# Kernel tuning notes

Measured on AMD Instinct MI355X. Metric: run time of the kernel, lower is better.

## Reference

```python
import jax, jax.numpy as jnp
import numpy as np

B, S, H, T, NF = 64, 512, 1024, 4, 12
P = NF * (NF - 1) // 2  # 66 step pairs


def _head(x, w1, b1, w2, b2):
    # LinearsHead (eval mode: dropout = identity): linear -> relu -> linear
    return jax.nn.relu(x @ w1 + b1) @ w2 + b2


def setup_inputs() -> dict:
    key = jax.random.key(0)
    ks = jax.random.split(key, 12)
    sc = 0.02
    # non-overlapping contiguous spans: targets then facts, each L tokens
    L = S // (T + NF)  # 32
    t_start = jnp.arange(T, dtype=jnp.int32) * L
    f_start = (T + jnp.arange(NF, dtype=jnp.int32)) * L
    target_offsets = jnp.broadcast_to(jnp.stack([t_start, t_start + L], -1), (B, T, 2))
    fact_offsets = jnp.broadcast_to(jnp.stack([f_start, f_start + L], -1), (B, NF, 2))
    return {
        'seq_features': jax.random.normal(ks[0], (B, S, H), jnp.float32),
        'cls_features': jax.random.normal(ks[1], (B, H), jnp.float32),
        'target_offsets': target_offsets,
        'fact_offsets': fact_offsets,
        'fact_score_mask': jnp.ones((B, NF, T), jnp.float32),
        'sentsim_w1': sc * jax.random.normal(ks[2], (2 * H, H), jnp.float32),
        'sentsim_b1': jnp.zeros((H,), jnp.float32),
        'sentsim_w2': sc * jax.random.normal(ks[3], (H, 1), jnp.float32),
        'sentsim_b2': jnp.zeros((1,), jnp.float32),
        'step_w1': sc * jax.random.normal(ks[4], (2 * H, H), jnp.float32),
        'step_b1': jnp.zeros((H,), jnp.float32),
        'step_w2': sc * jax.random.normal(ks[5], (H, 1), jnp.float32),
        'step_b2': jnp.zeros((1,), jnp.float32),
        'state_w1': sc * jax.random.normal(ks[6], (H, H), jnp.float32),
        'state_b1': jnp.zeros((H,), jnp.float32),
        'state_w2': sc * jax.random.normal(ks[7], (H, 1), jnp.float32),
        'state_b2': jnp.zeros((1,), jnp.float32),
        'abd_w1': sc * jax.random.normal(ks[8], (2 * H, H), jnp.float32),
        'abd_b1': jnp.zeros((H,), jnp.float32),
        'abd_w2': sc * jax.random.normal(ks[9], (H, 1), jnp.float32),
        'abd_b2': jnp.zeros((1,), jnp.float32),
        'lambda_weight': jnp.array([0.5, 0.5], jnp.float32),
    }


def reference(seq_features, cls_features, target_offsets, fact_offsets, fact_score_mask,
              sentsim_w1, sentsim_b1, sentsim_w2, sentsim_b2,
              step_w1, step_b1, step_w2, step_b2,
              state_w1, state_b1, state_w2, state_b2,
              abd_w1, abd_b1, abd_w2, abd_b2, lambda_weight):
    b, s, h = seq_features.shape
    t = target_offsets.shape[1]
    nf = fact_offsets.shape[1]
    pos = jnp.arange(s)

    def seg_mean(offs):  # offs [b,k,2] -> mean-pooled [b,k,h]
        m = ((pos >= offs[..., 0:1]) & (pos < offs[..., 1:2])).astype(seq_features.dtype)
        cnt = (offs[..., 1] - offs[..., 0]).astype(seq_features.dtype)[..., None]
        return jnp.einsum('bks,bsh->bkh', m, seq_features) / cnt

    tgt = seg_mean(target_offsets)  # [b,t,h]
    fct = seg_mean(fact_offsets)    # [b,nf,h]

    # fact-cls pairs ordered target-major: features[ti*nf+fi] = cat(fact, target)
    ff = jnp.broadcast_to(fct[:, None], (b, t, nf, h))
    tt = jnp.broadcast_to(tgt[:, :, None], (b, t, nf, h))
    pair = jnp.concatenate([ff, tt], -1).reshape(b, t * nf, 2 * h)
    fact_score = jax.nn.sigmoid(_head(pair, sentsim_w1, sentsim_b1, sentsim_w2, sentsim_b2)[..., 0])  # [b, t*nf]
    # original does .view(len(facts), len(targets)) on the flat t-major scores
    mat = fact_score.reshape(b, nf, t)
    max_per_fact = jnp.max(mat * fact_score_mask, axis=2)  # [b, nf]
    state_fact = jnp.mean(max_per_fact, axis=1)            # [b]
    state_cls = jax.nn.sigmoid(_head(cls_features, state_w1, state_b1, state_w2, state_b2)[..., 0])
    w = jax.nn.softmax(lambda_weight)
    state = w[0] * state_fact + w[1] * state_cls           # [b]

    # step pairs: combinations(range(nf), 2) == row-major triu indices
    i1, i2 = jnp.triu_indices(nf, k=1)
    step_feat = jnp.concatenate([fct[:, i1], fct[:, i2]], -1)  # [b,P,2h]
    step = _head(step_feat, step_w1, step_b1, step_w2, step_b2)[..., 0]  # [b,P]

    tside = jnp.mean(tgt, axis=1)  # sum/len over targets [b,h]
    abd_feat = jnp.concatenate([jnp.broadcast_to(tside[:, None], (b, nf, h)), fct], -1)
    abd = _head(abd_feat, abd_w1, abd_b1, abd_w2, abd_b2)[..., 0]  # [b,nf]

    # step_func == 'softmax_all': joint softmax over step + abd scores
    allsc = jax.nn.softmax(jnp.concatenate([step, abd], axis=1), axis=1)
    np_pairs = i1.shape[0]
    step, abd = allsc[:, :np_pairs], allsc[:, np_pairs:]

    # pack: [state | fact_score | step | step_abd]
    return jnp.concatenate([state[:, None], fact_score, step, abd], axis=1)
```

## Files before the change

kernel.cpp:

```cpp
#include <hip/hip_runtime.h>
#include <hip/hip_bf16.h>

#define B_    64
#define S_    512
#define H_    1024
#define HH_   (H_*H_)
#define T_    4
#define NF_   12
#define TNF_  48
#define NP_   66
#define OUTC_ 127

#define NSENT_ (B_*TNF_)
#define NSTEP_ (B_*NP_)
#define NABD_  (B_*NF_)
#define NCLS_  (B_)
#define NWAVES_ (NSENT_+NSTEP_+NABD_+NCLS_)

#define AROW_FCT   0
#define AROW_TGT   768
#define AROW_TSD   1024
#define AROW_CLS   1088
#define AROWS_PAD_ 1280

#define GROW_FSENT 0
#define GROW_S1    768
#define GROW_S2    1536
#define GROW_AF    2304
#define GROW_TSENT 3072
#define GROW_AT    3328
#define GROW_CLS   3392
#define GROWS_     3456

typedef __bf16 bf16x8 __attribute__((ext_vector_type(8)));
typedef float  f32x4  __attribute__((ext_vector_type(4)));
typedef __attribute__((address_space(1))) const unsigned int gcu32;
typedef __attribute__((address_space(3))) unsigned int lu32;

__device__ __forceinline__ ushort f2bf(float x) {
    union { float f; unsigned u; } c; c.f = x;
    unsigned r = c.u + 0x7fffu + ((c.u >> 16) & 1u);
    return (ushort)(r >> 16);
}
__device__ __forceinline__ float bflo(unsigned u) {
    union { unsigned u; float f; } c; c.u = u << 16; return c.f;
}
__device__ __forceinline__ float bfhi(unsigned u) {
    union { unsigned u; float f; } c; c.u = u & 0xffff0000u; return c.f;
}

__global__ __launch_bounds__(256) void prep_kernel(
    const float* __restrict__ seq, const int* __restrict__ toffs,
    const int* __restrict__ foffs, const float* __restrict__ cls,
    const float* __restrict__ sw1, const float* __restrict__ pw1,
    const float* __restrict__ aw1, const float* __restrict__ cw1,
    float* __restrict__ tgt32, ushort* __restrict__ Abf,
    ushort* __restrict__ Wt)
{
    int blk = blockIdx.x;
    int tid = threadIdx.x;

    if (blk < 1024) {
        int b = blk >> 4;
        int k = blk & 15;
        int start, end, arow;
        float* dst32 = nullptr;
        if (k < T_) {
            start = toffs[(b*T_ + k)*2];
            end   = toffs[(b*T_ + k)*2 + 1];
            dst32 = tgt32 + (size_t)(b*T_ + k) * H_;
            arow  = AROW_TGT + b*T_ + k;
        } else {
            int f = k - T_;
            start = foffs[(b*NF_ + f)*2];
            end   = foffs[(b*NF_ + f)*2 + 1];
            arow  = AROW_FCT + b*NF_ + f;
        }
        int h0 = tid * 4;
        const float* base = seq + ((size_t)b * S_ + start) * H_ + h0;
        float4 s = make_float4(0.f, 0.f, 0.f, 0.f);
        int n = end - start;
        #pragma unroll 4
        for (int r = 0; r < n; ++r) {
            float4 v = *(const float4*)(base + (size_t)r * H_);
            s.x += v.x; s.y += v.y; s.z += v.z; s.w += v.w;
        }
        float inv = 1.f / (float)n;
        s.x *= inv; s.y *= inv; s.z *= inv; s.w *= inv;
        if (dst32) *(float4*)(dst32 + h0) = s;
        ushort4 q; q.x = f2bf(s.x); q.y = f2bf(s.y); q.z = f2bf(s.z); q.w = f2bf(s.w);
        *(ushort4*)(Abf + (size_t)arow * H_ + h0) = q;
    } else if (blk < 1088) {
        int b = blk - 1024;
        int h0 = tid * 4;
        float4 c = *(const float4*)(cls + (size_t)b * H_ + h0);
        ushort4 qc; qc.x = f2bf(c.x); qc.y = f2bf(c.y); qc.z = f2bf(c.z); qc.w = f2bf(c.w);
        *(ushort4*)(Abf + (size_t)(AROW_CLS + b) * H_ + h0) = qc;
    } else {
        __shared__ float Tt[32][133];
        int idx2 = blk - 1088;
        int z = idx2 >> 8;
        int rem = idx2 & 255;
        int k0     = (rem >> 3) * 32;
        int nstrip = (rem & 7) * 128;
        const float* src;
        switch (z) {
            case 0: src = sw1; break;
            case 1: src = pw1; break;
            case 2: src = pw1 + HH_; break;
            case 3: src = aw1 + HH_; break;
            case 4: src = sw1 + HH_; break;
            case 5: src = aw1; break;
            default: src = cw1; break;
        }
        int ty = tid >> 3, tx = tid & 7;
        const float* rsrc = src + (size_t)(k0 + ty) * H_ + nstrip + tx*4;
        float4 v0 = *(const float4*)(rsrc);
        float4 v1 = *(const float4*)(rsrc + 32);
        float4 v2 = *(const float4*)(rsrc + 64);
        float4 v3 = *(const float4*)(rsrc + 96);
        float4 vv[4] = {v0, v1, v2, v3};
        #pragma unroll
        for (int i = 0; i < 4; ++i) {
            Tt[ty][i*32 + tx*4 + 0] = vv[i].x;
            Tt[ty][i*32 + tx*4 + 1] = vv[i].y;
            Tt[ty][i*32 + tx*4 + 2] = vv[i].z;
            Tt[ty][i*32 + tx*4 + 3] = vv[i].w;
        }
        __syncthreads();
        #pragma unroll
        for (int i = 0; i < 4; ++i) {
            int nx = i*32 + ty;
            ushort4 q;
            q.x = f2bf(Tt[tx*4 + 0][nx]);
            q.y = f2bf(Tt[tx*4 + 1][nx]);
            q.z = f2bf(Tt[tx*4 + 2][nx]);
            q.w = f2bf(Tt[tx*4 + 3][nx]);
            *(ushort4*)(Wt + (size_t)z * HH_
                        + (size_t)(nstrip + nx) * H_ + k0 + tx*4) = q;
        }
    }
}

__global__ __launch_bounds__(256) void tside_kernel(
    const float* __restrict__ tgt32, ushort* __restrict__ Abf)
{
    int b = blockIdx.x;
    int h0 = threadIdx.x * 4;
    float4 s = make_float4(0.f, 0.f, 0.f, 0.f);
    for (int t = 0; t < T_; ++t) {
        float4 v = *(const float4*)(tgt32 + (size_t)(b*T_ + t)*H_ + h0);
        s.x += v.x; s.y += v.y; s.z += v.z; s.w += v.w;
    }
    ushort4 q;
    q.x = f2bf(s.x*0.25f); q.y = f2bf(s.y*0.25f);
    q.z = f2bf(s.z*0.25f); q.w = f2bf(s.w*0.25f);
    *(ushort4*)(Abf + (size_t)(AROW_TSD + b) * H_ + h0) = q;
}

__global__ __launch_bounds__(256) void gemm_bf16_kernel(
    const ushort* __restrict__ Abf, const ushort* __restrict__ Wt,
    ushort* __restrict__ G)
{
    __shared__ __align__(16) ushort As[2][128*32];
    __shared__ __align__(16) ushort Bs[2][128*32];

    int bx = blockIdx.x;
    int arow_base, wsel, grow_base, m0, vrows;
    if (bx < 24)      { int j = bx / 6; int mt = bx % 6; arow_base = AROW_FCT;
                        wsel = j; grow_base = j * 768; m0 = mt * 128; vrows = 128; }
    else if (bx < 26) { arow_base = AROW_TGT; wsel = 4; grow_base = GROW_TSENT;
                        m0 = (bx - 24) * 128; vrows = 128; }
    else if (bx == 26){ arow_base = AROW_TSD; wsel = 5; grow_base = GROW_AT;
                        m0 = 0; vrows = 64; }
    else              { arow_base = AROW_CLS; wsel = 6; grow_base = GROW_CLS;
                        m0 = 0; vrows = 64; }

    const int tid  = threadIdx.x;
    const int lane = tid & 63;
    const int w    = tid >> 6;
    const int wr   = w >> 1, wc = w & 1;
    const int n0   = blockIdx.y * 128;

    const int srow = lane >> 2;
    const int scol = ((lane & 3) ^ ((lane >> 3) & 3)) * 8;
    const ushort* gA0 = Abf + (size_t)(arow_base + m0 + w*16 + srow) * H_ + scol;
    const ushort* gA1 = gA0 + (size_t)64 * H_;
    const ushort* gB0 = Wt + (size_t)wsel * HH_
                        + (size_t)(n0 + w*16 + srow) * H_ + scol;
    const ushort* gB1 = gB0 + (size_t)64 * H_;
    const int ldsA0 = (0*64 + w*16) * 32, ldsA1 = (1*64 + w*16) * 32;

    const int frr  = lane & 15;
    const int c0   = lane >> 4;
    const int swz  = (frr >> 1) & 3;
    const int offA = (wr*64 + frr) * 32 + (c0 ^ swz) * 8;
    const int offB = (wc*64 + frr) * 32 + (c0 ^ swz) * 8;

    f32x4 acc[4][4];
    #pragma unroll
    for (int i = 0; i < 4; ++i)
        #pragma unroll
        for (int j = 0; j < 4; ++j)
            acc[i][j] = (f32x4){0.f, 0.f, 0.f, 0.f};

    #define STAGE(buf, kstep) do {                                              \
        int kk_ = (kstep) < 32 ? (kstep) * 32 : 0;                              \
        __builtin_amdgcn_global_load_lds((gcu32*)(gA0 + kk_),                   \
            (lu32*)(As[buf] + ldsA0), 16, 0, 0);                                \
        __builtin_amdgcn_global_load_lds((gcu32*)(gA1 + kk_),                   \
            (lu32*)(As[buf] + ldsA1), 16, 0, 0);                                \
        __builtin_amdgcn_global_load_lds((gcu32*)(gB0 + kk_),                   \
            (lu32*)(Bs[buf] + ldsA0), 16, 0, 0);                                \
        __builtin_amdgcn_global_load_lds((gcu32*)(gB1 + kk_),                   \
            (lu32*)(Bs[buf] + ldsA1), 16, 0, 0);                                \
    } while (0)

    STAGE(0, 0);
    STAGE(1, 1);

    #pragma unroll 1
    for (int t = 0; t < 32; ++t) {
        const int cur = t & 1;
        asm volatile("s_waitcnt vmcnt(4)" ::: "memory");
        __builtin_amdgcn_s_barrier();
        __builtin_amdgcn_sched_barrier(0);

        const ushort* pa = As[cur] + offA;
        const ushort* pb = Bs[cur] + offB;
        bf16x8 a0 = *(const bf16x8*)(pa);
        bf16x8 a1 = *(const bf16x8*)(pa + 16*32);
        bf16x8 a2 = *(const bf16x8*)(pa + 32*32);
        bf16x8 a3 = *(const bf16x8*)(pa + 48*32);
        bf16x8 b0 = *(const bf16x8*)(pb);
        bf16x8 b1 = *(const bf16x8*)(pb + 16*32);
        bf16x8 b2 = *(const bf16x8*)(pb + 32*32);
        bf16x8 b3 = *(const bf16x8*)(pb + 48*32);

        asm volatile("s_waitcnt lgkmcnt(0)" ::: "memory");
        __builtin_amdgcn_s_barrier();
        __builtin_amdgcn_sched_barrier(0);

        if (t < 30) STAGE(cur, t + 2);

        bf16x8 av[4] = {a0, a1, a2, a3};
        bf16x8 bv[4] = {b0, b1, b2, b3};
        #pragma unroll
        for (int i = 0; i < 4; ++i)
            #pragma unroll
            for (int j = 0; j < 4; ++j)
                acc[i][j] = __builtin_amdgcn_mfma_f32_16x16x32_bf16(
                    av[i], bv[j], acc[i][j], 0, 0, 0);
    }
    #undef STAGE

    const int r0 = (lane >> 4) * 4;
    const int cc = lane & 15;
    #pragma unroll
    for (int i = 0; i < 4; ++i) {
        int lrow = wr*64 + i*16 + r0;
        if (lrow >= vrows) continue;
        #pragma unroll
        for (int r = 0; r < 4; ++r) {
            size_t gr = (size_t)(grow_base + m0 + lrow + r) * H_ + n0 + wc*64 + cc;
            #pragma unroll
            for (int j = 0; j < 4; ++j)
                G[gr + j*16] = f2bf(acc[i][j][r]);
        }
    }
}

__global__ __launch_bounds__(256) void combine_kernel(
    const ushort* __restrict__ G,
    const float* __restrict__ sb1, const float* __restrict__ sw2,
    const float* __restrict__ pb1, const float* __restrict__ pw2,
    const float* __restrict__ ab1, const float* __restrict__ aw2,
    const float* __restrict__ cb1, const float* __restrict__ cw2,
    float* __restrict__ ssent, float* __restrict__ sstep,
    float* __restrict__ sabd, float* __restrict__ scls)
{
    int wv = blockIdx.x * 4 + (threadIdx.x >> 6);
    int lane = threadIdx.x & 63;
    if (wv >= NWAVES_) return;

    const ushort *U, *V;
    const float *b1, *w2;
    float* outp;
    if (wv < NSENT_) {
        int b = wv / TNF_, q = wv % TNF_;
        int t = q / NF_, f = q % NF_;
        U = G + (size_t)(GROW_FSENT + b*NF_ + f) * H_;
        V = G + (size_t)(GROW_TSENT + b*T_ + t) * H_;
        b1 = sb1; w2 = sw2; outp = ssent + wv;
    } else if (wv < NSENT_ + NSTEP_) {
        int s = wv - NSENT_;
        int b = s / NP_, p = s % NP_;
        int i = 0, rem = p, cnt = NF_ - 1;
        while (rem >= cnt) { rem -= cnt; --cnt; ++i; }
        int j = i + 1 + rem;
        U = G + (size_t)(GROW_S1 + b*NF_ + i) * H_;
        V = G + (size_t)(GROW_S2 + b*NF_ + j) * H_;
        b1 = pb1; w2 = pw2; outp = sstep + s;
    } else if (wv < NSENT_ + NSTEP_ + NABD_) {
        int s = wv - NSENT_ - NSTEP_;
        int b = s / NF_, f = s % NF_;
        U = G + (size_t)(GROW_AT + b) * H_;
        V = G + (size_t)(GROW_AF + b*NF_ + f) * H_;
        b1 = ab1; w2 = aw2; outp = sabd + s;
    } else {
        int b = wv - NSENT_ - NSTEP_ - NABD_;
        U = G + (size_t)(GROW_CLS + b) * H_;
        V = nullptr;
        b1 = cb1; w2 = cw2; outp = scls + b;
    }

    float acc = 0.f;
    #pragma unroll
    for (int h = 0; h < 2; ++h) {
        int nb = h * 512 + lane * 8;
        uint4 uu = *(const uint4*)(U + nb);
        float us[8] = { bflo(uu.x), bfhi(uu.x), bflo(uu.y), bfhi(uu.y),
                        bflo(uu.z), bfhi(uu.z), bflo(uu.w), bfhi(uu.w) };
        if (V) {
            uint4 vv = *(const uint4*)(V + nb);
            us[0] += bflo(vv.x); us[1] += bfhi(vv.x);
            us[2] += bflo(vv.y); us[3] += bfhi(vv.y);
            us[4] += bflo(vv.z); us[5] += bfhi(vv.z);
            us[6] += bflo(vv.w); us[7] += bfhi(vv.w);
        }
        float4 bA = *(const float4*)(b1 + nb);
        float4 bB = *(const float4*)(b1 + nb + 4);
        float4 wA = *(const float4*)(w2 + nb);
        float4 wB = *(const float4*)(w2 + nb + 4);
        acc = fmaf(fmaxf(us[0] + bA.x, 0.f), wA.x, acc);
        acc = fmaf(fmaxf(us[1] + bA.y, 0.f), wA.y, acc);
        acc = fmaf(fmaxf(us[2] + bA.z, 0.f), wA.z, acc);
        acc = fmaf(fmaxf(us[3] + bA.w, 0.f), wA.w, acc);
        acc = fmaf(fmaxf(us[4] + bB.x, 0.f), wB.x, acc);
        acc = fmaf(fmaxf(us[5] + bB.y, 0.f), wB.y, acc);
        acc = fmaf(fmaxf(us[6] + bB.z, 0.f), wB.z, acc);
        acc = fmaf(fmaxf(us[7] + bB.w, 0.f), wB.w, acc);
    }
    #pragma unroll
    for (int msk = 1; msk < 64; msk <<= 1)
        acc += __shfl_xor(acc, msk);
    if (lane == 0) *outp = acc;
}

__global__ __launch_bounds__(128) void finalize_kernel(
    const float* __restrict__ s_sent, const float* __restrict__ s_step,
    const float* __restrict__ s_abd, const float* __restrict__ s_cls,
    const float* __restrict__ mask, const float* __restrict__ lam,
    const float* __restrict__ sent_b2, const float* __restrict__ step_b2,
    const float* __restrict__ state_b2, const float* __restrict__ abd_b2,
    float* __restrict__ out)
{
    int b = blockIdx.x;
    int tid = threadIdx.x;
    __shared__ float fs[TNF_];
    __shared__ float sc[NP_ + NF_];
    __shared__ float mpf[NF_];
    __shared__ float smax, ssum;

    if (tid < TNF_) {
        float v = 1.f / (1.f + expf(-(s_sent[b*TNF_ + tid] + sent_b2[0])));
        fs[tid] = v;
        out[(size_t)b*OUTC_ + 1 + tid] = v;
    }
    if (tid < NP_)
        sc[tid] = s_step[b*NP_ + tid] + step_b2[0];
    else if (tid < NP_ + NF_)
        sc[tid] = s_abd[b*NF_ + (tid - NP_)] + abd_b2[0];
    __syncthreads();

    if (tid < NF_) {
        float m = -1e30f;
        for (int j = 0; j < T_; ++j)
            m = fmaxf(m, fs[tid*T_ + j] * mask[((size_t)b*NF_ + tid)*T_ + j]);
        mpf[tid] = m;
    }
    __syncthreads();

    if (tid == 0) {
        float sf = 0.f;
        for (int i = 0; i < NF_; ++i) sf += mpf[i];
        sf *= (1.f / NF_);
        float scls2 = 1.f / (1.f + expf(-(s_cls[b] + state_b2[0])));
        float l0 = lam[0], l1 = lam[1];
        float mx = fmaxf(l0, l1);
        float e0 = expf(l0 - mx), e1 = expf(l1 - mx);
        float w0 = e0 / (e0 + e1);
        out[(size_t)b*OUTC_] = w0 * sf + (1.f - w0) * scls2;
        float m2 = -1e30f;
        for (int i = 0; i < NP_ + NF_; ++i) m2 = fmaxf(m2, sc[i]);
        smax = m2;
    }
    __syncthreads();
    if (tid < NP_ + NF_) sc[tid] = expf(sc[tid] - smax);
    __syncthreads();
    if (tid == 0) {
        float s2 = 0.f;
        for (int i = 0; i < NP_ + NF_; ++i) s2 += sc[i];
        ssum = s2;
    }
    __syncthreads();
    if (tid < NP_ + NF_)
        out[(size_t)b*OUTC_ + 1 + TNF_ + tid] = sc[tid] / ssum;
}

extern "C" void kernel_launch(void* const* d_in, const int* in_sizes, int n_in,
                              void* d_out, int out_size, void* d_ws, size_t ws_size,
                              hipStream_t stream)
{
    (void)in_sizes; (void)n_in; (void)out_size; (void)ws_size;
    const float* seq  = (const float*)d_in[0];
    const float* cls  = (const float*)d_in[1];
    const int*   toff = (const int*)d_in[2];
    const int*   foff = (const int*)d_in[3];
    const float* mask = (const float*)d_in[4];
    const float* sw1  = (const float*)d_in[5];
    const float* sb1  = (const float*)d_in[6];
    const float* sw2  = (const float*)d_in[7];
    const float* sb2  = (const float*)d_in[8];
    const float* pw1  = (const float*)d_in[9];
    const float* pb1  = (const float*)d_in[10];
    const float* pw2  = (const float*)d_in[11];
    const float* pb2  = (const float*)d_in[12];
    const float* cw1  = (const float*)d_in[13];
    const float* cb1  = (const float*)d_in[14];
    const float* cw2  = (const float*)d_in[15];
    const float* cb2  = (const float*)d_in[16];
    const float* aw1  = (const float*)d_in[17];
    const float* ab1  = (const float*)d_in[18];
    const float* aw2  = (const float*)d_in[19];
    const float* ab2  = (const float*)d_in[20];
    const float* lam  = (const float*)d_in[21];

    char* wsb = (char*)d_ws;
    float*  tgt32 = (float*)wsb;
    float*  ssent = (float*)(wsb + (1u<<20));
    float*  sstep = ssent + NSENT_;
    float*  sabd  = sstep + NSTEP_;
    float*  scls  = sabd + NABD_;
    ushort* Abf   = (ushort*)(wsb + (1u<<20) + 32768);
    ushort* Wt    = Abf + (size_t)AROWS_PAD_ * H_;
    ushort* G     = Wt + (size_t)7 * HH_;

    prep_kernel<<<2880, 256, 0, stream>>>(
        seq, toff, foff, cls, sw1, pw1, aw1, cw1, tgt32, Abf, Wt);

    tside_kernel<<<B_, 256, 0, stream>>>(tgt32, Abf);

    gemm_bf16_kernel<<<dim3(28, 8), 256, 0, stream>>>(Abf, Wt, G);

    combine_kernel<<<(NWAVES_ + 3) / 4, 256, 0, stream>>>(
        G, sb1, sw2, pb1, pw2, ab1, aw2, cb1, cw2,
        ssent, sstep, sabd, scls);

    finalize_kernel<<<B_, 128, 0, stream>>>(
        ssent, sstep, sabd, scls, mask, lam, sb2, pb2, cb2, ab2, (float*)d_out);
}
```

Baseline: 62.16 us.

## Enlarge GEMM tiles to 256x256 with 8 waves and 4-stage LDS pipeline

Each GEMM block now computes a 256x256 output tile with 512 threads (8 waves, each holding 128x64 of accumulators) instead of 128x128 with 256 threads. The LDS ring grows from double to quadruple buffering with three stages in flight, and the barrier count per k-step drops from two to one. The grid shrinks from 224 to 60 blocks, which raises operand reuse per block but leaves most CUs idle on a 256-CU part. It also increases register and LDS pressure, and the A buffer is padded so the larger tiles stay in bounds.

```diff
diff --git a/kernel.cpp b/kernel.cpp
--- a/kernel.cpp
+++ b/kernel.cpp
@@ -21,7 +21,7 @@
 #define AROW_TGT   768
 #define AROW_TSD   1024
 #define AROW_CLS   1088
-#define AROWS_PAD_ 1280
+#define AROWS_PAD_ 1536
 
 #define GROW_FSENT 0
 #define GROW_S1    768
@@ -158,111 +158,121 @@
     *(ushort4*)(Abf + (size_t)(AROW_TSD + b) * H_ + h0) = q;
 }
 
-__global__ __launch_bounds__(256) void gemm_bf16_kernel(
+__global__ __launch_bounds__(512, 2) void gemm_bf16_kernel(
     const ushort* __restrict__ Abf, const ushort* __restrict__ Wt,
     ushort* __restrict__ G)
 {
-    __shared__ __align__(16) ushort As[2][128*32];
-    __shared__ __align__(16) ushort Bs[2][128*32];
-
-    int bx = blockIdx.x;
-    int arow_base, wsel, grow_base, m0, vrows;
-    if (bx < 24)      { int j = bx / 6; int mt = bx % 6; arow_base = AROW_FCT;
-                        wsel = j; grow_base = j * 768; m0 = mt * 128; vrows = 128; }
-    else if (bx < 26) { arow_base = AROW_TGT; wsel = 4; grow_base = GROW_TSENT;
-                        m0 = (bx - 24) * 128; vrows = 128; }
-    else if (bx == 26){ arow_base = AROW_TSD; wsel = 5; grow_base = GROW_AT;
-                        m0 = 0; vrows = 64; }
-    else              { arow_base = AROW_CLS; wsel = 6; grow_base = GROW_CLS;
-                        m0 = 0; vrows = 64; }
+    __shared__ __align__(16) ushort As[4][256*32];
+    __shared__ __align__(16) ushort Bs[4][256*32];
+
+    const int bx = blockIdx.x;
+    int arow, wsel, grow, vrows;
+    if (bx < 12)      { int j = bx / 3, mt = bx % 3;
+                        arow = AROW_FCT + mt*256; wsel = j;
+                        grow = j*768 + mt*256; vrows = 256; }
+    else if (bx == 12){ arow = AROW_TGT; wsel = 4; grow = GROW_TSENT; vrows = 256; }
+    else if (bx == 13){ arow = AROW_TSD; wsel = 5; grow = GROW_AT;    vrows = 64; }
+    else              { arow = AROW_CLS; wsel = 6; grow = GROW_CLS;   vrows = 64; }
 
     const int tid  = threadIdx.x;
     const int lane = tid & 63;
     const int w    = tid >> 6;
-    const int wr   = w >> 1, wc = w & 1;
-    const int n0   = blockIdx.y * 128;
+    const int wr   = w >> 2;
+    const int wc   = w & 3;
+    const int n0   = blockIdx.y * 256;
 
     const int srow = lane >> 2;
-    const int scol = ((lane & 3) ^ ((lane >> 3) & 3)) * 8;
-    const ushort* gA0 = Abf + (size_t)(arow_base + m0 + w*16 + srow) * H_ + scol;
-    const ushort* gA1 = gA0 + (size_t)64 * H_;
+    const int scol = ((lane & 3) ^ ((srow >> 1) & 3)) * 8;
+    const ushort* gA0 = Abf + (size_t)(arow + w*32 + srow) * H_ + scol;
+    const ushort* gA1 = gA0 + (size_t)16 * H_;
     const ushort* gB0 = Wt + (size_t)wsel * HH_
-                        + (size_t)(n0 + w*16 + srow) * H_ + scol;
-    const ushort* gB1 = gB0 + (size_t)64 * H_;
-    const int ldsA0 = (0*64 + w*16) * 32, ldsA1 = (1*64 + w*16) * 32;
+                        + (size_t)(n0 + w*32 + srow) * H_ + scol;
+    const ushort* gB1 = gB0 + (size_t)16 * H_;
+    const int ldsW = w * 1024;
 
     const int frr  = lane & 15;
-    const int c0   = lane >> 4;
-    const int swz  = (frr >> 1) & 3;
-    const int offA = (wr*64 + frr) * 32 + (c0 ^ swz) * 8;
-    const int offB = (wc*64 + frr) * 32 + (c0 ^ swz) * 8;
-
-    f32x4 acc[4][4];
+    const int kg   = lane >> 4;
+    const int swz8 = (kg ^ ((frr >> 1) & 3)) * 8;
+
+    f32x4 acc[8][4];
     #pragma unroll
-    for (int i = 0; i < 4; ++i)
+    for (int i = 0; i < 8; ++i)
         #pragma unroll
         for (int j = 0; j < 4; ++j)
             acc[i][j] = (f32x4){0.f, 0.f, 0.f, 0.f};
 
     #define STAGE(buf, kstep) do {                                              \
-        int kk_ = (kstep) < 32 ? (kstep) * 32 : 0;                              \
+        int kk_ = (kstep) * 32;                                                 \
         __builtin_amdgcn_global_load_lds((gcu32*)(gA0 + kk_),                   \
-            (lu32*)(As[buf] + ldsA0), 16, 0, 0);                                \
+            (lu32*)(As[buf] + ldsW), 16, 0, 0);                                 \
         __builtin_amdgcn_global_load_lds((gcu32*)(gA1 + kk_),                   \
-            (lu32*)(As[buf] + ldsA1), 16, 0, 0);                                \
+            (lu32*)(As[buf] + ldsW + 512), 16, 0, 0);                           \
         __builtin_amdgcn_global_load_lds((gcu32*)(gB0 + kk_),                   \
-            (lu32*)(Bs[buf] + ldsA0), 16, 0, 0);                                \
+            (lu32*)(Bs[buf] + ldsW), 16, 0, 0);                                 \
         __builtin_amdgcn_global_load_lds((gcu32*)(gB1 + kk_),                   \
-            (lu32*)(Bs[buf] + ldsA1), 16, 0, 0);                                \
+            (lu32*)(Bs[buf] + ldsW + 512), 16, 0, 0);                           \
+    } while (0)
+
+    #define COMPUTE(cur) do {                                                   \
+        const ushort* pa = As[cur];                                             \
+        const ushort* pb = Bs[cur];                                             \
+        bf16x8 av0 = *(const bf16x8*)(pa + (wr*128 + 0*16 + frr)*32 + swz8);    \
+        bf16x8 av1 = *(const bf16x8*)(pa + (wr*128 + 1*16 + frr)*32 + swz8);    \
+        bf16x8 av2 = *(const bf16x8*)(pa + (wr*128 + 2*16 + frr)*32 + swz8);    \
+        bf16x8 av3 = *(const bf16x8*)(pa + (wr*128 + 3*16 + frr)*32 + swz8);    \
+        bf16x8 av4 = *(const bf16x8*)(pa + (wr*128 + 4*16 + frr)*32 + swz8);    \
+        bf16x8 av5 = *(const bf16x8*)(pa + (wr*128 + 5*16 + frr)*32 + swz8);    \
+        bf16x8 av6 = *(const bf16x8*)(pa + (wr*128 + 6*16 + frr)*32 + swz8);    \
+        bf16x8 av7 = *(const bf16x8*)(pa + (wr*128 + 7*16 + frr)*32 + swz8);    \
+        bf16x8 bv0 = *(const bf16x8*)(pb + (wc*64 + 0*16 + frr)*32 + swz8);     \
+        bf16x8 bv1 = *(const bf16x8*)(pb + (wc*64 + 1*16 + frr)*32 + swz8);     \
+        bf16x8 bv2 = *(const bf16x8*)(pb + (wc*64 + 2*16 + frr)*32 + swz8);     \
+        bf16x8 bv3 = *(const bf16x8*)(pb + (wc*64 + 3*16 + frr)*32 + swz8);     \
+        asm volatile("s_waitcnt lgkmcnt(0)" ::: "memory");                      \
+        __builtin_amdgcn_sched_barrier(0);                                      \
+        bf16x8 av[8] = {av0, av1, av2, av3, av4, av5, av6, av7};                \
+        bf16x8 bv[4] = {bv0, bv1, bv2, bv3};                                    \
+        _Pragma("unroll")                                                       \
+        for (int i = 0; i < 8; ++i)                                             \
+            _Pragma("unroll")                                                   \
+            for (int j = 0; j < 4; ++j)                                         \
+                acc[i][j] = __builtin_amdgcn_mfma_f32_16x16x32_bf16(            \
+                    av[i], bv[j], acc[i][j], 0, 0, 0);                          \
     } while (0)
 
     STAGE(0, 0);
     STAGE(1, 1);
+    STAGE(2, 2);
 
     #pragma unroll 1
-    for (int t = 0; t < 32; ++t) {
-        const int cur = t & 1;
-        asm volatile("s_waitcnt vmcnt(4)" ::: "memory");
+    for (int t = 0; t < 30; ++t) {
+        asm volatile("s_waitcnt vmcnt(8)" ::: "memory");
         __builtin_amdgcn_s_barrier();
         __builtin_amdgcn_sched_barrier(0);
-
-        const ushort* pa = As[cur] + offA;
-        const ushort* pb = Bs[cur] + offB;
-        bf16x8 a0 = *(const bf16x8*)(pa);
-        bf16x8 a1 = *(const bf16x8*)(pa + 16*32);
-        bf16x8 a2 = *(const bf16x8*)(pa + 32*32);
-        bf16x8 a3 = *(const bf16x8*)(pa + 48*32);
-        bf16x8 b0 = *(const bf16x8*)(pb);
-        bf16x8 b1 = *(const bf16x8*)(pb + 16*32);
-        bf16x8 b2 = *(const bf16x8*)(pb + 32*32);
-        bf16x8 b3 = *(const bf16x8*)(pb + 48*32);
-
-        asm volatile("s_waitcnt lgkmcnt(0)" ::: "memory");
-        __builtin_amdgcn_s_barrier();
-        __builtin_amdgcn_sched_barrier(0);
-
-        if (t < 30) STAGE(cur, t + 2);
-
-        bf16x8 av[4] = {a0, a1, a2, a3};
-        bf16x8 bv[4] = {b0, b1, b2, b3};
-        #pragma unroll
-        for (int i = 0; i < 4; ++i)
-            #pragma unroll
-            for (int j = 0; j < 4; ++j)
-                acc[i][j] = __builtin_amdgcn_mfma_f32_16x16x32_bf16(
-                    av[i], bv[j], acc[i][j], 0, 0, 0);
-    }
+        if (t < 29) STAGE((t + 3) & 3, t + 3);
+        COMPUTE(t & 3);
+    }
+    asm volatile("s_waitcnt vmcnt(4)" ::: "memory");
+    __builtin_amdgcn_s_barrier();
+    __builtin_amdgcn_sched_barrier(0);
+    COMPUTE(2);
+    asm volatile("s_waitcnt vmcnt(0)" ::: "memory");
+    __builtin_amdgcn_s_barrier();
+    __builtin_amdgcn_sched_barrier(0);
+    COMPUTE(3);
+
     #undef STAGE
+    #undef COMPUTE
 
     const int r0 = (lane >> 4) * 4;
     const int cc = lane & 15;
     #pragma unroll
-    for (int i = 0; i < 4; ++i) {
-        int lrow = wr*64 + i*16 + r0;
+    for (int i = 0; i < 8; ++i) {
+        int lrow = wr*128 + i*16 + r0;
         if (lrow >= vrows) continue;
         #pragma unroll
         for (int r = 0; r < 4; ++r) {
-            size_t gr = (size_t)(grow_base + m0 + lrow + r) * H_ + n0 + wc*64 + cc;
+            size_t gr = (size_t)(grow + lrow + r) * H_ + n0 + wc*64 + cc;
             #pragma unroll
             for (int j = 0; j < 4; ++j)
                 G[gr + j*16] = f2bf(acc[i][j][r]);
@@ -451,7 +461,7 @@
 
     tside_kernel<<<B_, 256, 0, stream>>>(tgt32, Abf);
 
-    gemm_bf16_kernel<<<dim3(28, 8), 256, 0, stream>>>(Abf, Wt, G);
+    gemm_bf16_kernel<<<dim3(15, 4), 512, 0, stream>>>(Abf, Wt, G);
 
     combine_kernel<<<(NWAVES_ + 3) / 4, 256, 0, stream>>>(
         G, sb1, sw2, pb1, pw2, ab1, aw2, cb1, cw2,
```

Result: slower. 82.06 us (+32.0%).
